# Performance work log

Measured on AMD Instinct MI355X. Metric: run time of the kernel, lower is better.

The kernel has to match this reference:

```python
import jax, jax.numpy as jnp
import numpy as np

B, D = 32768, 1024


def setup_inputs() -> dict:
    key = jax.random.key(0)
    kx, k1, k2, k3 = jax.random.split(key, 4)
    x = jax.random.normal(kx, (B, D), dtype=jnp.float32)
    w1 = jax.random.normal(k1, (D, D), dtype=jnp.float32) * 0.1
    w2 = jax.random.normal(k2, (D, D), dtype=jnp.float32) * 0.1
    w3 = jax.random.normal(k3, (D, D), dtype=jnp.float32) * 0.1
    return {"x": x, "w1": w1, "w2": w2, "w3": w3}


def reference(x, w1, w2, w3):
    # Order 1: plain dense projection
    r1 = jnp.matmul(x, w1)  # [B, D]

    dim = x.shape[1]
    k = int(dim * 0.1)
    # Select top-k facets by mean |x| over the batch
    _, idx = jax.lax.top_k(jnp.abs(x).mean(axis=0), k)  # [k]
    mask = jnp.zeros((dim,), dtype=x.dtype).at[idx].set(1.0)  # [D]

    x_sparse = x * mask  # [B, D], zero outside active facets
    # Order 2: masked matmul, gated elementwise by the sparse input
    r2 = jnp.matmul(x_sparse, w2) * x_sparse
    # Order 3: masked matmul squared, gated elementwise
    r3 = jnp.square(jnp.matmul(x_sparse, w3)) * x_sparse
    return (r1, r2, r3)
```

## Files before the change

### kernel.cpp

```cpp
#include <hip/hip_runtime.h>
#include <hip/hip_bf16.h>
#include <stdint.h>

#define B_ROWS 32768
#define DIM    1024
#define KACT   102
#define KPAD   104

typedef short bf16x8 __attribute__((ext_vector_type(8)));
typedef unsigned short u16x8 __attribute__((ext_vector_type(8)));
typedef float f32x4  __attribute__((ext_vector_type(4)));

__device__ __forceinline__ unsigned short f2bf(float f) {
  union { float f; unsigned u; } v; v.f = f;
  unsigned u = v.u;
  unsigned r = u + 0x7fffu + ((u >> 16) & 1u);
  return (unsigned short)(r >> 16);
}
__device__ __forceinline__ float bfasf(unsigned hi16) {
  union { unsigned u; float f; } v; v.u = hi16;
  return v.f;
}

#define GLDS(g, l) __builtin_amdgcn_global_load_lds( \
    (__attribute__((address_space(1))) void*)(g),    \
    (__attribute__((address_space(3))) void*)(l), 16, 0, 0)

__global__ __launch_bounds__(256) void k_convw(
    const float* __restrict__ x, const float* __restrict__ w1,
    unsigned short* __restrict__ xb, unsigned short* __restrict__ w1t,
    float* __restrict__ partial) {
  const int t = threadIdx.x;
  if (blockIdx.x < 512) {
    const int c0 = t * 4;
    const size_t base = (size_t)blockIdx.x * 64 * DIM;
    float s0 = 0.f, s1 = 0.f, s2 = 0.f, s3 = 0.f;
    #pragma unroll 4
    for (int j = 0; j < 64; ++j) {
      size_t off = base + (size_t)j * DIM + c0;
      float4 v = *(const float4*)(x + off);
      s0 += fabsf(v.x); s1 += fabsf(v.y); s2 += fabsf(v.z); s3 += fabsf(v.w);
      ushort4 o;
      o.x = f2bf(v.x); o.y = f2bf(v.y); o.z = f2bf(v.z); o.w = f2bf(v.w);
      *(ushort4*)(xb + off) = o;
    }
    float4 p; p.x = s0; p.y = s1; p.z = s2; p.w = s3;
    *(float4*)(partial + (size_t)blockIdx.x * DIM + c0) = p;
  } else {
    __shared__ unsigned short tile[64][65];
    const int b  = blockIdx.x - 512;
    const int bx = b & 15;
    const int by = b >> 4;
    for (int e = t; e < 64 * 64; e += 256) {
      int r = e >> 6, c = e & 63;
      tile[r][c] = f2bf(w1[(size_t)(by * 64 + r) * DIM + bx * 64 + c]);
    }
    __syncthreads();
    for (int e = t; e < 64 * 64; e += 256) {
      int c = e >> 6, r = e & 63;
      w1t[(size_t)(bx * 64 + c) * DIM + by * 64 + r] = tile[r][c];
    }
  }
}

__global__ __launch_bounds__(128) void k_reduce1(const float* __restrict__ partial,
                                                 float* __restrict__ p2) {
  const int c  = (blockIdx.x & 7) * 128 + threadIdx.x;
  const int ks = blockIdx.x >> 3;
  float s = 0.f;
  #pragma unroll 8
  for (int p = ks * 64; p < ks * 64 + 64; ++p) s += partial[(size_t)p * DIM + c];
  p2[ks * DIM + c] = s;
}

__global__ __launch_bounds__(1024) void k_sel(const float* __restrict__ p2,
                                              int* __restrict__ act,
                                              int* __restrict__ cmap) {
  __shared__ double sv[DIM];
  __shared__ int wcnt[16];
  const int d = threadIdx.x;
  {
    double s = 0.0;
    #pragma unroll
    for (int ks = 0; ks < 8; ++ks) s += (double)p2[ks * DIM + d];
    sv[d] = s;
  }
  __syncthreads();
  const double sd = sv[d];
  int rank = 0;
  for (int j = 0; j < DIM; ++j) {
    double s = sv[j];
    rank += (s > sd || (s == sd && j < d)) ? 1 : 0;
  }
  const int f = (rank < KACT) ? 1 : 0;
  unsigned long long m = __ballot(f != 0);
  const int lane = d & 63, w = d >> 6;
  if (lane == 0) wcnt[w] = __popcll(m);
  __syncthreads();
  int off = 0;
  for (int i = 0; i < w; ++i) off += wcnt[i];
  int pos = off + __popcll(m & ((1ull << lane) - 1ull));
  cmap[d] = f ? pos : -1;
  if (f) act[pos] = d;
}

__global__ __launch_bounds__(128) void k_wsub(const float* __restrict__ w2,
                                              const float* __restrict__ w3,
                                              const int* __restrict__ act,
                                              float* __restrict__ W2sub,
                                              float* __restrict__ W3sub) {
  const int i = blockIdx.x;
  const int j = threadIdx.x;
  if (j >= KPAD) return;
  float v2 = 0.f, v3 = 0.f;
  if (i < KACT && j < KACT) {
    size_t o = (size_t)act[i] * DIM + act[j];
    v2 = w2[o]; v3 = w3[o];
  }
  W2sub[i * KPAD + j] = v2;
  W3sub[i * KPAD + j] = v3;
}

#define VMW4 asm volatile("s_waitcnt vmcnt(4)" ::: "memory")
#define VMW0 asm volatile("s_waitcnt vmcnt(0)" ::: "memory")
#define NOP_ (void)0

#define STAGE_A(KT) do { \
  GLDS(Abase + (size_t)sr0 * 1024 + (KT) * 32 + sc0 * 8, &Asl[((KT)&3)*8192 + p0*8]); \
  GLDS(Abase + (size_t)sr1 * 1024 + (KT) * 32 + sc1 * 8, &Asl[((KT)&3)*8192 + p1*8]); \
} while (0)
#define STAGE_B(KT) do { \
  GLDS(Bbase + (size_t)sr0 * 1024 + (KT) * 32 + sc0 * 8, &Bsl[((KT)&3)*8192 + p0*8]); \
  GLDS(Bbase + (size_t)sr1 * 1024 + (KT) * 32 + sc1 * 8, &Bsl[((KT)&3)*8192 + p1*8]); \
} while (0)

#define PH0(SLOT, STAGE_STMT) do { \
  _Pragma("unroll") for (int i = 0; i < 4; ++i) \
    areg[i] = *(const bf16x8*)(&Asl[(SLOT)*8192 + aoff0 + i * 512]); \
  _Pragma("unroll") for (int i = 0; i < 4; ++i) \
    breg[i] = *(const bf16x8*)(&Bsl[(SLOT)*8192 + boff0 + i * 512]); \
  STAGE_STMT; \
  __builtin_amdgcn_s_barrier(); \
  __builtin_amdgcn_s_setprio(1); \
  _Pragma("unroll") for (int mi = 0; mi < 4; ++mi) \
  _Pragma("unroll") for (int ni = 0; ni < 4; ++ni) \
    acc[mi][ni] = __builtin_amdgcn_mfma_f32_16x16x32_bf16(areg[mi], breg[ni], acc[mi][ni], 0, 0, 0); \
  __builtin_amdgcn_s_setprio(0); \
  __builtin_amdgcn_s_barrier(); \
} while (0)

#define PH1(SLOT, STAGE_STMT, WAIT_STMT) do { \
  _Pragma("unroll") for (int i = 0; i < 4; ++i) \
    areg[i] = *(const bf16x8*)(&Asl[(SLOT)*8192 + aoff0 + 2048 + i * 512]); \
  STAGE_STMT; \
  WAIT_STMT; \
  __builtin_amdgcn_s_barrier(); \
  __builtin_amdgcn_s_setprio(1); \
  _Pragma("unroll") for (int mi = 0; mi < 4; ++mi) \
  _Pragma("unroll") for (int ni = 0; ni < 4; ++ni) \
    acc[4 + mi][ni] = __builtin_amdgcn_mfma_f32_16x16x32_bf16(areg[mi], breg[ni], acc[4 + mi][ni], 0, 0, 0); \
  __builtin_amdgcn_s_setprio(0); \
  __builtin_amdgcn_s_barrier(); \
} while (0)

__global__ __launch_bounds__(512, 1) void k_gemm_r1(
    const unsigned short* __restrict__ A,
    const unsigned short* __restrict__ Bt,
    float* __restrict__ C) {
  __shared__ unsigned short Asl[4 * 8192];
  __shared__ unsigned short Bsl[4 * 8192];

  const int t    = threadIdx.x;
  const int lane = t & 63;
  const int wave = t >> 6;
  const int wm   = wave >> 2;
  const int wn   = wave & 3;
  const int la   = lane & 15;
  const int kg   = lane >> 4;
  const int kgx  = kg ^ ((la >> 1) & 3);

  const int swz  = (blockIdx.x & 7) * 64 + (blockIdx.x >> 3);
  const int brow = swz >> 2;
  const int bcol = swz & 3;

  const unsigned short* Abase = A  + (size_t)brow * 256 * 1024;
  const unsigned short* Bbase = Bt + (size_t)bcol * 256 * 1024;

  const int p0 = t, p1 = t + 512;
  const int q0 = p0 ^ ((p0 >> 3) & 3);
  const int q1 = p1 ^ ((p1 >> 3) & 3);
  const int sr0 = q0 >> 2, sc0 = q0 & 3;
  const int sr1 = q1 >> 2, sc1 = q1 & 3;

  const int aoff0 = (wm * 128 + la) * 32 + kgx * 8;
  const int boff0 = (wn * 64  + la) * 32 + kgx * 8;

  f32x4 acc[8][4];
  #pragma unroll
  for (int mi = 0; mi < 8; ++mi)
    #pragma unroll
    for (int ni = 0; ni < 4; ++ni)
      acc[mi][ni] = (f32x4){0.f, 0.f, 0.f, 0.f};

  bf16x8 areg[4], breg[4];

  STAGE_A(0); STAGE_B(0); STAGE_A(1); STAGE_B(1);
  VMW4;
  __builtin_amdgcn_s_barrier();

  for (int kt4 = 0; kt4 < 28; kt4 += 4) {
    PH0(0, STAGE_A(kt4 + 2)); PH1(0, STAGE_B(kt4 + 2), VMW4);
    PH0(1, STAGE_A(kt4 + 3)); PH1(1, STAGE_B(kt4 + 3), VMW4);
    PH0(2, STAGE_A(kt4 + 4)); PH1(2, STAGE_B(kt4 + 4), VMW4);
    PH0(3, STAGE_A(kt4 + 5)); PH1(3, STAGE_B(kt4 + 5), VMW4);
  }
  PH0(0, STAGE_A(30)); PH1(0, STAGE_B(30), VMW4);
  PH0(1, STAGE_A(31)); PH1(1, STAGE_B(31), VMW4);
  PH0(2, NOP_);        PH1(2, NOP_, VMW0);
  PH0(3, NOP_);        PH1(3, NOP_, NOP_);

  const int orow0 = brow * 256 + wm * 128 + (lane >> 4) * 4;
  const int ocol0 = bcol * 256 + wn * 64 + la;
  #pragma unroll
  for (int mi = 0; mi < 8; ++mi)
    #pragma unroll
    for (int ni = 0; ni < 4; ++ni)
      #pragma unroll
      for (int r = 0; r < 4; ++r)
        C[(size_t)(orow0 + mi * 16 + r) * DIM + ocol0 + ni * 16] = acc[mi][ni][r];
}

__global__ __launch_bounds__(512) void k_r23(
    const unsigned short* __restrict__ xb,
    const float* __restrict__ W2sub,
    const float* __restrict__ W3sub,
    const int* __restrict__ cmap,
    float* __restrict__ out2,
    float* __restrict__ out3) {
  __shared__ float W2s[KPAD * KPAD];
  __shared__ float W3s[KPAD * KPAD];
  __shared__ float xs[2][16 * KPAD];
  __shared__ float r2s[16 * KPAD];
  __shared__ float r3s[16 * KPAD];
  __shared__ int   cms[DIM];
  const int t    = threadIdx.x;
  const int row0 = blockIdx.x * 128;

  for (int e = t; e < KPAD * KPAD; e += 512) { W2s[e] = W2sub[e]; W3s[e] = W3sub[e]; }
  for (int e = t; e < DIM; e += 512) cms[e] = cmap[e];
  for (int e = t; e < 2 * 16 * KPAD; e += 512) ((float*)xs)[e] = 0.f;
  __syncthreads();

  const int  j   = t & 127;
  const int  rg  = (t >> 7) & 3;
  const bool jok = j < KACT;

  auto LOADR = [&](int ch, u16x8* ld) {
    const size_t base = (size_t)(row0 + ch * 16) * DIM;
    #pragma unroll
    for (int it = 0; it < 4; ++it) {
      int e = t + it * 512;
      int r = e >> 7, c8 = e & 127;
      ld[it] = *(const u16x8*)(xb + base + (size_t)r * DIM + c8 * 8);
    }
  };
  auto XSW = [&](int buf, const u16x8* ld) {
    #pragma unroll
    for (int it = 0; it < 4; ++it) {
      int e = t + it * 512;
      int r = e >> 7, c8 = e & 127;
      #pragma unroll
      for (int q = 0; q < 8; ++q) {
        int m = cms[c8 * 8 + q];
        if (m >= 0) xs[buf][r * KPAD + m] = bfasf(((unsigned)(unsigned short)ld[it][q]) << 16);
      }
    }
  };
  auto COMPUTE = [&](int buf) {
    if (jok) {
      float a2[4], a3[4];
      #pragma unroll
      for (int r = 0; r < 4; ++r) { a2[r] = 0.f; a3[r] = 0.f; }
      for (int i = 0; i < KPAD; i += 4) {
        float w2v[4], w3v[4];
        #pragma unroll
        for (int q = 0; q < 4; ++q) {
          w2v[q] = W2s[(i + q) * KPAD + j];
          w3v[q] = W3s[(i + q) * KPAD + j];
        }
        #pragma unroll
        for (int r = 0; r < 4; ++r) {
          f32x4 xv = *(const f32x4*)(&xs[buf][(rg * 4 + r) * KPAD + i]);
          a2[r] += xv[0] * w2v[0] + xv[1] * w2v[1] + xv[2] * w2v[2] + xv[3] * w2v[3];
          a3[r] += xv[0] * w3v[0] + xv[1] * w3v[1] + xv[2] * w3v[2] + xv[3] * w3v[3];
        }
      }
      #pragma unroll
      for (int r = 0; r < 4; ++r) {
        int rr = rg * 4 + r;
        float g = xs[buf][rr * KPAD + j];
        r2s[rr * KPAD + j] = a2[r] * g;
        r3s[rr * KPAD + j] = a3[r] * a3[r] * g;
      }
    }
  };
  auto WRITEOUT = [&](int ch) {
    const int r0 = row0 + ch * 16;
    const int c0 = (t & 255) * 4;
    const int rh = t >> 8;
    const int4 cm = *(const int4*)(&cms[c0]);
    #pragma unroll
    for (int k = 0; k < 8; ++k) {
      int r = rh + k * 2;
      const float* rr2 = &r2s[r * KPAD];
      const float* rr3 = &r3s[r * KPAD];
      float4 o2, o3;
      o2.x = (cm.x >= 0) ? rr2[cm.x] : 0.f;  o3.x = (cm.x >= 0) ? rr3[cm.x] : 0.f;
      o2.y = (cm.y >= 0) ? rr2[cm.y] : 0.f;  o3.y = (cm.y >= 0) ? rr3[cm.y] : 0.f;
      o2.z = (cm.z >= 0) ? rr2[cm.z] : 0.f;  o3.z = (cm.z >= 0) ? rr3[cm.z] : 0.f;
      o2.w = (cm.w >= 0) ? rr2[cm.w] : 0.f;  o3.w = (cm.w >= 0) ? rr3[cm.w] : 0.f;
      size_t oo = (size_t)(r0 + r) * DIM + c0;
      *(float4*)(out2 + oo) = o2;
      *(float4*)(out3 + oo) = o3;
    }
  };

  u16x8 ldA[4], ldB[4];
  LOADR(0, ldA);
  XSW(0, ldA);
  __syncthreads();
  for (int ch2 = 0; ch2 < 8; ch2 += 2) {
    if (ch2 + 1 < 8) LOADR(ch2 + 1, ldB);
    COMPUTE(0);
    __syncthreads();
    WRITEOUT(ch2);
    if (ch2 + 1 < 8) XSW(1, ldB);
    __syncthreads();
    if (ch2 + 2 < 8) LOADR(ch2 + 2, ldA);
    COMPUTE(1);
    __syncthreads();
    WRITEOUT(ch2 + 1);
    if (ch2 + 2 < 8) XSW(0, ldA);
    __syncthreads();
  }
}

extern "C" void kernel_launch(void* const* d_in, const int* in_sizes, int n_in,
                              void* d_out, int out_size, void* d_ws, size_t ws_size,
                              hipStream_t stream) {
  const float* x  = (const float*)d_in[0];
  const float* w1 = (const float*)d_in[1];
  const float* w2 = (const float*)d_in[2];
  const float* w3 = (const float*)d_in[3];

  float* out1 = (float*)d_out;
  float* out2 = out1 + (size_t)B_ROWS * DIM;
  float* out3 = out2 + (size_t)B_ROWS * DIM;

  char* ws = (char*)d_ws;
  unsigned short* xb     = (unsigned short*)ws;
  unsigned short* w1t    = (unsigned short*)(ws + 67108864);
  float*          partial= (float*)(ws + 69206016);
  float*          p2     = (float*)(ws + 71303168);
  int*            cmap   = (int*)(ws + 71335936);
  int*            act    = (int*)(ws + 71340032);
  float*          W2sub  = (float*)(ws + 71340544);
  float*          W3sub  = (float*)(ws + 71383808);

  k_convw   <<<dim3(768),  dim3(256),  0, stream>>>(x, w1, xb, w1t, partial);
  k_reduce1 <<<dim3(64),   dim3(128),  0, stream>>>(partial, p2);
  k_sel     <<<dim3(1),    dim3(1024), 0, stream>>>(p2, act, cmap);
  k_wsub    <<<dim3(KPAD), dim3(128),  0, stream>>>(w2, w3, act, W2sub, W3sub);
  k_gemm_r1 <<<dim3(512),  dim3(512),  0, stream>>>(xb, w1t, out1);
  k_r23     <<<dim3(256),  dim3(512),  0, stream>>>(xb, W2sub, W3sub, cmap, out2, out3);
}
```

Before: 254.1 us.

## Fuse dense GEMM and sparse r2/r3 kernels into one interleaved launch

Merges the r1 GEMM kernel and the r2/r3 masked-matmul kernel into a single 768-block launch. Every third group of 8 blocks runs the r2/r3 path and the rest run the GEMM path, sharing one 128KB dynamic-style smem buffer. The aim is to overlap the write-bandwidth-bound r2/r3 work with the compute-bound GEMM and to remove one launch boundary and its tail. In exchange, every block now reserves the larger shared-memory footprint, and register pressure is set by the heavier GEMM path.

```diff
diff --git a/kernel.cpp b/kernel.cpp
--- a/kernel.cpp
+++ b/kernel.cpp
@@ -163,185 +163,193 @@
   __builtin_amdgcn_s_barrier(); \
 } while (0)
 
-__global__ __launch_bounds__(512, 1) void k_gemm_r1(
+__global__ __launch_bounds__(512, 1) void k_fused(
     const unsigned short* __restrict__ A,
     const unsigned short* __restrict__ Bt,
-    float* __restrict__ C) {
-  __shared__ unsigned short Asl[4 * 8192];
-  __shared__ unsigned short Bsl[4 * 8192];
-
-  const int t    = threadIdx.x;
-  const int lane = t & 63;
-  const int wave = t >> 6;
-  const int wm   = wave >> 2;
-  const int wn   = wave & 3;
-  const int la   = lane & 15;
-  const int kg   = lane >> 4;
-  const int kgx  = kg ^ ((la >> 1) & 3);
-
-  const int swz  = (blockIdx.x & 7) * 64 + (blockIdx.x >> 3);
-  const int brow = swz >> 2;
-  const int bcol = swz & 3;
-
-  const unsigned short* Abase = A  + (size_t)brow * 256 * 1024;
-  const unsigned short* Bbase = Bt + (size_t)bcol * 256 * 1024;
-
-  const int p0 = t, p1 = t + 512;
-  const int q0 = p0 ^ ((p0 >> 3) & 3);
-  const int q1 = p1 ^ ((p1 >> 3) & 3);
-  const int sr0 = q0 >> 2, sc0 = q0 & 3;
-  const int sr1 = q1 >> 2, sc1 = q1 & 3;
-
-  const int aoff0 = (wm * 128 + la) * 32 + kgx * 8;
-  const int boff0 = (wn * 64  + la) * 32 + kgx * 8;
-
-  f32x4 acc[8][4];
-  #pragma unroll
-  for (int mi = 0; mi < 8; ++mi)
-    #pragma unroll
-    for (int ni = 0; ni < 4; ++ni)
-      acc[mi][ni] = (f32x4){0.f, 0.f, 0.f, 0.f};
-
-  bf16x8 areg[4], breg[4];
-
-  STAGE_A(0); STAGE_B(0); STAGE_A(1); STAGE_B(1);
-  VMW4;
-  __builtin_amdgcn_s_barrier();
-
-  for (int kt4 = 0; kt4 < 28; kt4 += 4) {
-    PH0(0, STAGE_A(kt4 + 2)); PH1(0, STAGE_B(kt4 + 2), VMW4);
-    PH0(1, STAGE_A(kt4 + 3)); PH1(1, STAGE_B(kt4 + 3), VMW4);
-    PH0(2, STAGE_A(kt4 + 4)); PH1(2, STAGE_B(kt4 + 4), VMW4);
-    PH0(3, STAGE_A(kt4 + 5)); PH1(3, STAGE_B(kt4 + 5), VMW4);
-  }
-  PH0(0, STAGE_A(30)); PH1(0, STAGE_B(30), VMW4);
-  PH0(1, STAGE_A(31)); PH1(1, STAGE_B(31), VMW4);
-  PH0(2, NOP_);        PH1(2, NOP_, VMW0);
-  PH0(3, NOP_);        PH1(3, NOP_, NOP_);
-
-  const int orow0 = brow * 256 + wm * 128 + (lane >> 4) * 4;
-  const int ocol0 = bcol * 256 + wn * 64 + la;
-  #pragma unroll
-  for (int mi = 0; mi < 8; ++mi)
-    #pragma unroll
-    for (int ni = 0; ni < 4; ++ni)
-      #pragma unroll
-      for (int r = 0; r < 4; ++r)
-        C[(size_t)(orow0 + mi * 16 + r) * DIM + ocol0 + ni * 16] = acc[mi][ni][r];
-}
-
-__global__ __launch_bounds__(512) void k_r23(
-    const unsigned short* __restrict__ xb,
+    float* __restrict__ C,
     const float* __restrict__ W2sub,
     const float* __restrict__ W3sub,
     const int* __restrict__ cmap,
     float* __restrict__ out2,
     float* __restrict__ out3) {
-  __shared__ float W2s[KPAD * KPAD];
-  __shared__ float W3s[KPAD * KPAD];
-  __shared__ float xs[2][16 * KPAD];
-  __shared__ float r2s[16 * KPAD];
-  __shared__ float r3s[16 * KPAD];
-  __shared__ int   cms[DIM];
-  const int t    = threadIdx.x;
-  const int row0 = blockIdx.x * 128;
-
-  for (int e = t; e < KPAD * KPAD; e += 512) { W2s[e] = W2sub[e]; W3s[e] = W3sub[e]; }
-  for (int e = t; e < DIM; e += 512) cms[e] = cmap[e];
-  for (int e = t; e < 2 * 16 * KPAD; e += 512) ((float*)xs)[e] = 0.f;
-  __syncthreads();
-
-  const int  j   = t & 127;
-  const int  rg  = (t >> 7) & 3;
-  const bool jok = j < KACT;
-
-  auto LOADR = [&](int ch, u16x8* ld) {
-    const size_t base = (size_t)(row0 + ch * 16) * DIM;
+  __shared__ __align__(16) char smem[131072];
+  const int t = threadIdx.x;
+  const int G = blockIdx.x >> 3;
+
+  if ((G % 3) != 1) {
+    const int Gg       = G - (G + 1) / 3;
+    const int gemm_ord = Gg * 8 + (blockIdx.x & 7);
+
+    unsigned short* Asl = (unsigned short*)smem;
+    unsigned short* Bsl = (unsigned short*)(smem + 65536);
+
+    const int lane = t & 63;
+    const int wave = t >> 6;
+    const int wm   = wave >> 2;
+    const int wn   = wave & 3;
+    const int la   = lane & 15;
+    const int kg   = lane >> 4;
+    const int kgx  = kg ^ ((la >> 1) & 3);
+
+    const int swz  = (gemm_ord & 7) * 64 + (gemm_ord >> 3);
+    const int brow = swz >> 2;
+    const int bcol = swz & 3;
+
+    const unsigned short* Abase = A  + (size_t)brow * 256 * 1024;
+    const unsigned short* Bbase = Bt + (size_t)bcol * 256 * 1024;
+
+    const int p0 = t, p1 = t + 512;
+    const int q0 = p0 ^ ((p0 >> 3) & 3);
+    const int q1 = p1 ^ ((p1 >> 3) & 3);
+    const int sr0 = q0 >> 2, sc0 = q0 & 3;
+    const int sr1 = q1 >> 2, sc1 = q1 & 3;
+
+    const int aoff0 = (wm * 128 + la) * 32 + kgx * 8;
+    const int boff0 = (wn * 64  + la) * 32 + kgx * 8;
+
+    f32x4 acc[8][4];
     #pragma unroll
-    for (int it = 0; it < 4; ++it) {
-      int e = t + it * 512;
-      int r = e >> 7, c8 = e & 127;
-      ld[it] = *(const u16x8*)(xb + base + (size_t)r * DIM + c8 * 8);
-    }
-  };
-  auto XSW = [&](int buf, const u16x8* ld) {
+    for (int mi = 0; mi < 8; ++mi)
+      #pragma unroll
+      for (int ni = 0; ni < 4; ++ni)
+        acc[mi][ni] = (f32x4){0.f, 0.f, 0.f, 0.f};
+
+    bf16x8 areg[4], breg[4];
+
+    STAGE_A(0); STAGE_B(0); STAGE_A(1); STAGE_B(1);
+    VMW4;
+    __builtin_amdgcn_s_barrier();
+
+    for (int kt4 = 0; kt4 < 28; kt4 += 4) {
+      PH0(0, STAGE_A(kt4 + 2)); PH1(0, STAGE_B(kt4 + 2), VMW4);
+      PH0(1, STAGE_A(kt4 + 3)); PH1(1, STAGE_B(kt4 + 3), VMW4);
+      PH0(2, STAGE_A(kt4 + 4)); PH1(2, STAGE_B(kt4 + 4), VMW4);
+      PH0(3, STAGE_A(kt4 + 5)); PH1(3, STAGE_B(kt4 + 5), VMW4);
+    }
+    PH0(0, STAGE_A(30)); PH1(0, STAGE_B(30), VMW4);
+    PH0(1, STAGE_A(31)); PH1(1, STAGE_B(31), VMW4);
+    PH0(2, NOP_);        PH1(2, NOP_, VMW0);
+    PH0(3, NOP_);        PH1(3, NOP_, NOP_);
+
+    const int orow0 = brow * 256 + wm * 128 + (lane >> 4) * 4;
+    const int ocol0 = bcol * 256 + wn * 64 + la;
     #pragma unroll
-    for (int it = 0; it < 4; ++it) {
-      int e = t + it * 512;
-      int r = e >> 7, c8 = e & 127;
-      #pragma unroll
-      for (int q = 0; q < 8; ++q) {
-        int m = cms[c8 * 8 + q];
-        if (m >= 0) xs[buf][r * KPAD + m] = bfasf(((unsigned)(unsigned short)ld[it][q]) << 16);
+    for (int mi = 0; mi < 8; ++mi)
+      #pragma unroll
+      for (int ni = 0; ni < 4; ++ni)
+        #pragma unroll
+        for (int r = 0; r < 4; ++r)
+          C[(size_t)(orow0 + mi * 16 + r) * DIM + ocol0 + ni * 16] = acc[mi][ni][r];
+  } else {
+    const int r23_ord = ((G - 1) / 3) * 8 + (blockIdx.x & 7);
+    const int row0 = r23_ord * 128;
+
+    float* W2s = (float*)smem;
+    float* W3s = (float*)(smem + 43264);
+    float* xs0 = (float*)(smem + 86528);
+    float* r2s = (float*)(smem + 99840);
+    float* r3s = (float*)(smem + 106496);
+    int*   cms = (int*)  (smem + 113152);
+
+    for (int e = t; e < KPAD * KPAD; e += 512) { W2s[e] = W2sub[e]; W3s[e] = W3sub[e]; }
+    for (int e = t; e < DIM; e += 512) cms[e] = cmap[e];
+    for (int e = t; e < 2 * 16 * KPAD; e += 512) xs0[e] = 0.f;
+    __syncthreads();
+
+    const int  j   = t & 127;
+    const int  rg  = (t >> 7) & 3;
+    const bool jok = j < KACT;
+
+    auto LOADR = [&](int ch, u16x8* ld) {
+      const size_t base = (size_t)(row0 + ch * 16) * DIM;
+      #pragma unroll
+      for (int it = 0; it < 4; ++it) {
+        int e = t + it * 512;
+        int r = e >> 7, c8 = e & 127;
+        ld[it] = *(const u16x8*)(A + base + (size_t)r * DIM + c8 * 8);
       }
-    }
-  };
-  auto COMPUTE = [&](int buf) {
-    if (jok) {
-      float a2[4], a3[4];
-      #pragma unroll
-      for (int r = 0; r < 4; ++r) { a2[r] = 0.f; a3[r] = 0.f; }
-      for (int i = 0; i < KPAD; i += 4) {
-        float w2v[4], w3v[4];
+    };
+    auto XSW = [&](int buf, const u16x8* ld) {
+      float* xsb = xs0 + buf * (16 * KPAD);
+      #pragma unroll
+      for (int it = 0; it < 4; ++it) {
+        int e = t + it * 512;
+        int r = e >> 7, c8 = e & 127;
         #pragma unroll
-        for (int q = 0; q < 4; ++q) {
-          w2v[q] = W2s[(i + q) * KPAD + j];
-          w3v[q] = W3s[(i + q) * KPAD + j];
+        for (int q = 0; q < 8; ++q) {
+          int m = cms[c8 * 8 + q];
+          if (m >= 0) xsb[r * KPAD + m] = bfasf(((unsigned)(unsigned short)ld[it][q]) << 16);
+        }
+      }
+    };
+    auto COMPUTE = [&](int buf) {
+      float* xsb = xs0 + buf * (16 * KPAD);
+      if (jok) {
+        float a2[4], a3[4];
+        #pragma unroll
+        for (int r = 0; r < 4; ++r) { a2[r] = 0.f; a3[r] = 0.f; }
+        for (int i = 0; i < KPAD; i += 4) {
+          float w2v[4], w3v[4];
+          #pragma unroll
+          for (int q = 0; q < 4; ++q) {
+            w2v[q] = W2s[(i + q) * KPAD + j];
+            w3v[q] = W3s[(i + q) * KPAD + j];
+          }
+          #pragma unroll
+          for (int r = 0; r < 4; ++r) {
+            f32x4 xv = *(const f32x4*)(&xsb[(rg * 4 + r) * KPAD + i]);
+            a2[r] += xv[0] * w2v[0] + xv[1] * w2v[1] + xv[2] * w2v[2] + xv[3] * w2v[3];
+            a3[r] += xv[0] * w3v[0] + xv[1] * w3v[1] + xv[2] * w3v[2] + xv[3] * w3v[3];
+          }
         }
         #pragma unroll
         for (int r = 0; r < 4; ++r) {
-          f32x4 xv = *(const f32x4*)(&xs[buf][(rg * 4 + r) * KPAD + i]);
-          a2[r] += xv[0] * w2v[0] + xv[1] * w2v[1] + xv[2] * w2v[2] + xv[3] * w2v[3];
-          a3[r] += xv[0] * w3v[0] + xv[1] * w3v[1] + xv[2] * w3v[2] + xv[3] * w3v[3];
+          int rr = rg * 4 + r;
+          float g = xsb[rr * KPAD + j];
+          r2s[rr * KPAD + j] = a2[r] * g;
+          r3s[rr * KPAD + j] = a3[r] * a3[r] * g;
         }
       }
-      #pragma unroll
-      for (int r = 0; r < 4; ++r) {
-        int rr = rg * 4 + r;
-        float g = xs[buf][rr * KPAD + j];
-        r2s[rr * KPAD + j] = a2[r] * g;
-        r3s[rr * KPAD + j] = a3[r] * a3[r] * g;
+    };
+    auto WRITEOUT = [&](int ch) {
+      const int r0 = row0 + ch * 16;
+      const int c0 = (t & 255) * 4;
+      const int rh = t >> 8;
+      const int4 cm = *(const int4*)(&cms[c0]);
+      #pragma unroll
+      for (int k = 0; k < 8; ++k) {
+        int r = rh + k * 2;
+        const float* rr2 = &r2s[r * KPAD];
+        const float* rr3 = &r3s[r * KPAD];
+        float4 o2, o3;
+        o2.x = (cm.x >= 0) ? rr2[cm.x] : 0.f;  o3.x = (cm.x >= 0) ? rr3[cm.x] : 0.f;
+        o2.y = (cm.y >= 0) ? rr2[cm.y] : 0.f;  o3.y = (cm.y >= 0) ? rr3[cm.y] : 0.f;
+        o2.z = (cm.z >= 0) ? rr2[cm.z] : 0.f;  o3.z = (cm.z >= 0) ? rr3[cm.z] : 0.f;
+        o2.w = (cm.w >= 0) ? rr2[cm.w] : 0.f;  o3.w = (cm.w >= 0) ? rr3[cm.w] : 0.f;
+        size_t oo = (size_t)(r0 + r) * DIM + c0;
+        *(float4*)(out2 + oo) = o2;
+        *(float4*)(out3 + oo) = o3;
       }
-    }
-  };
-  auto WRITEOUT = [&](int ch) {
-    const int r0 = row0 + ch * 16;
-    const int c0 = (t & 255) * 4;
-    const int rh = t >> 8;
-    const int4 cm = *(const int4*)(&cms[c0]);
-    #pragma unroll
-    for (int k = 0; k < 8; ++k) {
-      int r = rh + k * 2;
-      const float* rr2 = &r2s[r * KPAD];
-      const float* rr3 = &r3s[r * KPAD];
-      float4 o2, o3;
-      o2.x = (cm.x >= 0) ? rr2[cm.x] : 0.f;  o3.x = (cm.x >= 0) ? rr3[cm.x] : 0.f;
-      o2.y = (cm.y >= 0) ? rr2[cm.y] : 0.f;  o3.y = (cm.y >= 0) ? rr3[cm.y] : 0.f;
-      o2.z = (cm.z >= 0) ? rr2[cm.z] : 0.f;  o3.z = (cm.z >= 0) ? rr3[cm.z] : 0.f;
-      o2.w = (cm.w >= 0) ? rr2[cm.w] : 0.f;  o3.w = (cm.w >= 0) ? rr3[cm.w] : 0.f;
-      size_t oo = (size_t)(r0 + r) * DIM + c0;
-      *(float4*)(out2 + oo) = o2;
-      *(float4*)(out3 + oo) = o3;
-    }
-  };
-
-  u16x8 ldA[4], ldB[4];
-  LOADR(0, ldA);
-  XSW(0, ldA);
-  __syncthreads();
-  for (int ch2 = 0; ch2 < 8; ch2 += 2) {
-    if (ch2 + 1 < 8) LOADR(ch2 + 1, ldB);
-    COMPUTE(0);
+    };
+
+    u16x8 ldA[4], ldB[4];
+    LOADR(0, ldA);
+    XSW(0, ldA);
     __syncthreads();
-    WRITEOUT(ch2);
-    if (ch2 + 1 < 8) XSW(1, ldB);
-    __syncthreads();
-    if (ch2 + 2 < 8) LOADR(ch2 + 2, ldA);
-    COMPUTE(1);
-    __syncthreads();
-    WRITEOUT(ch2 + 1);
-    if (ch2 + 2 < 8) XSW(0, ldA);
-    __syncthreads();
+    for (int ch2 = 0; ch2 < 8; ch2 += 2) {
+      if (ch2 + 1 < 8) LOADR(ch2 + 1, ldB);
+      COMPUTE(0);
+      __syncthreads();
+      WRITEOUT(ch2);
+      if (ch2 + 1 < 8) XSW(1, ldB);
+      __syncthreads();
+      if (ch2 + 2 < 8) LOADR(ch2 + 2, ldA);
+      COMPUTE(1);
+      __syncthreads();
+      WRITEOUT(ch2 + 1);
+      if (ch2 + 2 < 8) XSW(0, ldA);
+      __syncthreads();
+    }
   }
 }
 
@@ -371,6 +379,6 @@
   k_reduce1 <<<dim3(64),   dim3(128),  0, stream>>>(partial, p2);
   k_sel     <<<dim3(1),    dim3(1024), 0, stream>>>(p2, act, cmap);
   k_wsub    <<<dim3(KPAD), dim3(128),  0, stream>>>(w2, w3, act, W2sub, W3sub);
-  k_gemm_r1 <<<dim3(512),  dim3(512),  0, stream>>>(xb, w1t, out1);
-  k_r23     <<<dim3(256),  dim3(512),  0, stream>>>(xb, W2sub, W3sub, cmap, out2, out3);
-}
+  k_fused   <<<dim3(768),  dim3(512),  0, stream>>>(xb, w1t, out1, W2sub, W3sub,
+                                                    cmap, out2, out3);
+}
```

Measured after the change: 281.9 us. 1.11x slower.
